# Optimization experiments

Measured on AMD Instinct MI355X. Metric: run time of the kernel, lower is better.

## Reference

```python
import jax, jax.numpy as jnp
import numpy as np

N, INC, INN, OUTC, OUTN, MAXD = 16, 32, 65536, 32, 8192, 16

def setup_inputs() -> dict:
    key = jax.random.key(0)
    ks = jax.random.split(key, 7)
    x = jax.random.normal(ks[0], (N, INC, INN), jnp.float32)
    A = jax.random.randint(ks[1], (OUTN, MAXD), 0, INN, dtype=jnp.int64)
    weight = 0.2 * jax.random.normal(ks[2], (INC, INN), jnp.float32)
    # normalize=True with fixed degree MAXD -> mask = 1/maxD everywhere
    mask = jnp.ones((OUTN, MAXD, 1), jnp.float32) / MAXD
    mask_weight = 0.2 * jax.random.normal(ks[3], (OUTN, MAXD, 1), jnp.float32)
    ct_weight = jax.random.normal(ks[4], (OUTC, INC), jnp.float32) / np.sqrt(INC)
    ct_bias = 0.02 * jax.random.normal(ks[5], (OUTC,), jnp.float32)
    bias = 0.2 * jax.random.normal(ks[6], (OUTC, OUTN), jnp.float32)
    return {"x": x, "A": A, "weight": weight, "mask": mask,
            "mask_weight": mask_weight, "ct_weight": ct_weight,
            "ct_bias": ct_bias, "bias": bias}

def reference(x, A, weight, mask, mask_weight, ct_weight, ct_bias, bias):
    n, inc, inn = x.shape
    outn, maxD = A.shape
    # per-input-node channel scaling, then lay out as (inn, N*inc) feature table
    feat = (x * weight).reshape(n * inc, inn).T            # (inn, N*inc)
    emb = feat[A]                                          # (outn, maxD, N*inc) gather
    w = mask_weight * mask                                 # (outn, maxD, 1)
    pooled = (w * emb).reshape(outn, maxD, n, inc).sum(axis=1)  # (outn, N, inc)
    almost_y = jnp.einsum('onc,dc->ond', pooled, ct_weight) + ct_bias  # (outn, N, outc)
    return almost_y.transpose(1, 2, 0) + bias              # (N, outc, outn)
```

## Files before the change

### kernel.cpp

```cpp
#include <hip/hip_runtime.h>
#include <hip/hip_bf16.h>

#define NN    16
#define INC   32
#define INN   65536
#define OUTC  32
#define OUTN  8192
#define MAXD  16
#define NC    512

typedef __attribute__((ext_vector_type(8))) unsigned short ushort8;
typedef __attribute__((ext_vector_type(4))) float f32x4;

__global__ __launch_bounds__(256) void transpose_scale_kernel(
    const float* __restrict__ x,
    const float* __restrict__ weight,
    unsigned short* __restrict__ feat)
{
    __shared__ float tile[64][65];
    const int l  = threadIdx.x;
    const int j0 = blockIdx.x * 64;
    const int r0 = blockIdx.y * 64;

    #pragma unroll
    for (int it = 0; it < 4; ++it) {
        int idx = it * 256 + l;
        int rl  = idx >> 4;
        int jj  = idx & 15;
        int r   = r0 + rl;
        int c   = r & 31;
        int j   = j0 + jj * 4;
        f32x4 xv = __builtin_nontemporal_load(
            reinterpret_cast<const f32x4*>(x + (size_t)r * INN + j));
        f32x4 wv = *reinterpret_cast<const f32x4*>(weight + (size_t)c * INN + j);
        tile[jj * 4 + 0][rl] = xv[0] * wv[0];
        tile[jj * 4 + 1][rl] = xv[1] * wv[1];
        tile[jj * 4 + 2][rl] = xv[2] * wv[2];
        tile[jj * 4 + 3][rl] = xv[3] * wv[3];
    }
    __syncthreads();

    #pragma unroll
    for (int p = 0; p < 2; ++p) {
        int jl = p * 32 + (l >> 3);
        int rs = (l & 7) * 8;
        ushort8 pk;
        #pragma unroll
        for (int k = 0; k < 8; ++k) {
            float v = tile[jl][rs + k];
            pk[k] = __bfloat16_as_ushort(__float2bfloat16(v));
        }
        *reinterpret_cast<ushort8*>(
            feat + (size_t)(j0 + jl) * NC + r0 + rs) = pk;
    }
}

#define OTILE 16

__global__ __launch_bounds__(512, 4) void gather_gemm_kernel(
    const unsigned short* __restrict__ feat,
    const int*   __restrict__ A,
    const float* __restrict__ mask,
    const float* __restrict__ mw,
    const float* __restrict__ ctw,
    const float* __restrict__ ctb,
    const float* __restrict__ bias,
    float*       __restrict__ out)
{
    __shared__ float pooled[OTILE][NC];
    __shared__ int   A_l[OTILE * MAXD];
    __shared__ float w_l[OTILE * MAXD];
    __shared__ float bias_l[32 * OTILE];

    const int l    = threadIdx.x;
    const int wave = l >> 6;
    const int lane = l & 63;
    const int o0   = blockIdx.x * OTILE;

    if (l < OTILE * MAXD) {
        A_l[l] = A[o0 * MAXD + l] & (INN - 1);
        w_l[l] = mw[o0 * MAXD + l] * mask[o0 * MAXD + l];
    }
    {
        int dout = l >> 4, o = l & 15;
        bias_l[l] = bias[(size_t)dout * OUTN + o0 + o];
    }
    __syncthreads();

    #pragma unroll
    for (int i = 0; i < 2; ++i) {
        const int o = wave + 8 * i;
        float acc[8] = {0.f, 0.f, 0.f, 0.f, 0.f, 0.f, 0.f, 0.f};
        #pragma unroll
        for (int d = 0; d < MAXD; ++d) {
            int   j  = A_l[o * MAXD + d];
            float wv = w_l[o * MAXD + d];
            ushort8 p = *reinterpret_cast<const ushort8*>(
                feat + (size_t)j * NC + lane * 8);
            #pragma unroll
            for (int k = 0; k < 8; ++k)
                acc[k] += wv * __uint_as_float((unsigned)p[k] << 16);
        }
        *reinterpret_cast<f32x4*>(&pooled[o][lane * 4]) =
            f32x4{acc[0], acc[1], acc[2], acc[3]};
        *reinterpret_cast<f32x4*>(&pooled[o][256 + lane * 4]) =
            f32x4{acc[4], acc[5], acc[6], acc[7]};
    }
    __syncthreads();

    const int dout = l & 31;
    const int n    = l >> 5;
    const float cb = ctb[dout];
    float vals[OTILE];
    #pragma unroll
    for (int o = 0; o < OTILE; ++o) vals[o] = cb + bias_l[dout * OTILE + o];

    #pragma unroll
    for (int q = 0; q < 8; ++q) {
        f32x4 cw = *reinterpret_cast<const f32x4*>(ctw + dout * 32 + 4 * q);
        const int sbase = (q & 1) * 256 + n * 16 + 4 * (q >> 1);
        #pragma unroll
        for (int o = 0; o < OTILE; ++o) {
            f32x4 pv = *reinterpret_cast<const f32x4*>(&pooled[o][sbase]);
            vals[o] += pv[0] * cw[0] + pv[1] * cw[1] + pv[2] * cw[2] + pv[3] * cw[3];
        }
    }

    float* orow = out + ((size_t)(n * 32 + dout)) * OUTN + o0;
    #pragma unroll
    for (int qq = 0; qq < 4; ++qq) {
        __builtin_nontemporal_store(
            f32x4{vals[4*qq], vals[4*qq+1], vals[4*qq+2], vals[4*qq+3]},
            reinterpret_cast<f32x4*>(orow + 4 * qq));
    }
}

extern "C" void kernel_launch(void* const* d_in, const int* in_sizes, int n_in,
                              void* d_out, int out_size, void* d_ws, size_t ws_size,
                              hipStream_t stream)
{
    const float* x      = (const float*)d_in[0];
    const int*   A      = (const int*)  d_in[1];
    const float* weight = (const float*)d_in[2];
    const float* mask   = (const float*)d_in[3];
    const float* mw     = (const float*)d_in[4];
    const float* ctw    = (const float*)d_in[5];
    const float* ctb    = (const float*)d_in[6];
    const float* bias   = (const float*)d_in[7];
    float* out = (float*)d_out;

    unsigned short* feat = (unsigned short*)d_ws;

    dim3 gA(INN / 64, NC / 64);
    transpose_scale_kernel<<<gA, 256, 0, stream>>>(x, weight, feat);

    gather_gemm_kernel<<<OUTN / OTILE, 512, 0, stream>>>(
        feat, A, mask, mw, ctw, ctb, bias, out);
}
```

Before: 258.8 us.

## Fuse transpose and gather-GEMM into one cooperative kernel with grid sync

Merges the transpose/scale pass and the gather-pool-GEMM pass into a single persistent cooperative kernel of 256 blocks. A grid-wide sync separates the two phases, and the two phases share one LDS union. The aim is to remove the second kernel launch and the gap between launches. In exchange the grid is much smaller, with one block per CU and 512 threads, so there is less latency hiding than the original 8192-block grid had. The two-kernel path is kept as a fallback if the cooperative launch fails.

```diff
diff --git a/kernel.cpp b/kernel.cpp
--- a/kernel.cpp
+++ b/kernel.cpp
@@ -1,5 +1,8 @@
 #include <hip/hip_runtime.h>
 #include <hip/hip_bf16.h>
+#include <hip/hip_cooperative_groups.h>
+
+namespace cg = cooperative_groups;
 
 #define NN    16
 #define INC   32
@@ -8,9 +11,145 @@
 #define OUTN  8192
 #define MAXD  16
 #define NC    512
+#define OTILE 16
+#define NBLK  256
 
 typedef __attribute__((ext_vector_type(8))) unsigned short ushort8;
 typedef __attribute__((ext_vector_type(4))) float f32x4;
+
+struct SMem {
+    union {
+        float tile[64][65];
+        float pooled[OTILE][NC];
+    } u;
+    int   A_l[OTILE * MAXD];
+    float w_l[OTILE * MAXD];
+    float bias_l[32 * OTILE];
+};
+
+__global__ __launch_bounds__(512, 2) void fused_kernel(
+    const float* __restrict__ x,
+    const float* __restrict__ weight,
+    const int*   __restrict__ A,
+    const float* __restrict__ mask,
+    const float* __restrict__ mw,
+    const float* __restrict__ ctw,
+    const float* __restrict__ ctb,
+    const float* __restrict__ bias,
+    unsigned short* __restrict__ feat,
+    float*       __restrict__ out)
+{
+    __shared__ SMem s;
+    const int l    = threadIdx.x;
+    const int bid  = blockIdx.x;
+    const int wave = l >> 6;
+    const int lane = l & 63;
+
+    #pragma unroll
+    for (int jt = 0; jt < 4; ++jt) {
+        const int j0 = bid * 256 + jt * 64;
+        for (int rc = 0; rc < 8; ++rc) {
+            const int r0 = rc * 64;
+            #pragma unroll
+            for (int it = 0; it < 2; ++it) {
+                int idx = it * 512 + l;
+                int rl  = idx >> 4;
+                int jj  = idx & 15;
+                int r   = r0 + rl;
+                int c   = r & 31;
+                int j   = j0 + jj * 4;
+                f32x4 xv = __builtin_nontemporal_load(
+                    reinterpret_cast<const f32x4*>(x + (size_t)r * INN + j));
+                f32x4 wv = *reinterpret_cast<const f32x4*>(
+                    weight + (size_t)c * INN + j);
+                s.u.tile[jj * 4 + 0][rl] = xv[0] * wv[0];
+                s.u.tile[jj * 4 + 1][rl] = xv[1] * wv[1];
+                s.u.tile[jj * 4 + 2][rl] = xv[2] * wv[2];
+                s.u.tile[jj * 4 + 3][rl] = xv[3] * wv[3];
+            }
+            __syncthreads();
+            {
+                int jl = l >> 3;
+                int rs = (l & 7) * 8;
+                ushort8 pk;
+                #pragma unroll
+                for (int k = 0; k < 8; ++k) {
+                    float v = s.u.tile[jl][rs + k];
+                    pk[k] = __bfloat16_as_ushort(__float2bfloat16(v));
+                }
+                *reinterpret_cast<ushort8*>(
+                    feat + (size_t)(j0 + jl) * NC + r0 + rs) = pk;
+            }
+            __syncthreads();
+        }
+    }
+
+    __threadfence();
+    cg::this_grid().sync();
+
+    for (int g = 0; g < 2; ++g) {
+        const int o0 = bid * 32 + g * OTILE;
+
+        if (l < OTILE * MAXD) {
+            s.A_l[l] = A[o0 * MAXD + l] & (INN - 1);
+            s.w_l[l] = mw[o0 * MAXD + l] * mask[o0 * MAXD + l];
+        }
+        {
+            int dout = l >> 4, o = l & 15;
+            s.bias_l[l] = bias[(size_t)dout * OUTN + o0 + o];
+        }
+        __syncthreads();
+
+        #pragma unroll
+        for (int i = 0; i < 2; ++i) {
+            const int o = wave + 8 * i;
+            float acc[8] = {0.f, 0.f, 0.f, 0.f, 0.f, 0.f, 0.f, 0.f};
+            #pragma unroll
+            for (int d = 0; d < MAXD; ++d) {
+                int   j  = s.A_l[o * MAXD + d];
+                float wv = s.w_l[o * MAXD + d];
+                ushort8 p = *reinterpret_cast<const ushort8*>(
+                    feat + (size_t)j * NC + lane * 8);
+                #pragma unroll
+                for (int k = 0; k < 8; ++k)
+                    acc[k] += wv * __uint_as_float((unsigned)p[k] << 16);
+            }
+            *reinterpret_cast<f32x4*>(&s.u.pooled[o][lane * 4]) =
+                f32x4{acc[0], acc[1], acc[2], acc[3]};
+            *reinterpret_cast<f32x4*>(&s.u.pooled[o][256 + lane * 4]) =
+                f32x4{acc[4], acc[5], acc[6], acc[7]};
+        }
+        __syncthreads();
+
+        const int dout = l & 31;
+        const int n    = l >> 5;
+        const float cb = ctb[dout];
+        float vals[OTILE];
+        #pragma unroll
+        for (int o = 0; o < OTILE; ++o)
+            vals[o] = cb + s.bias_l[dout * OTILE + o];
+
+        #pragma unroll
+        for (int q = 0; q < 8; ++q) {
+            f32x4 cw = *reinterpret_cast<const f32x4*>(ctw + dout * 32 + 4 * q);
+            const int sbase = (q & 1) * 256 + n * 16 + 4 * (q >> 1);
+            #pragma unroll
+            for (int o = 0; o < OTILE; ++o) {
+                f32x4 pv = *reinterpret_cast<const f32x4*>(&s.u.pooled[o][sbase]);
+                vals[o] += pv[0]*cw[0] + pv[1]*cw[1] + pv[2]*cw[2] + pv[3]*cw[3];
+            }
+        }
+
+        float* orow = out + ((size_t)(n * 32 + dout)) * OUTN + o0;
+        #pragma unroll
+        for (int qq = 0; qq < 4; ++qq) {
+            __builtin_nontemporal_store(
+                f32x4{vals[4*qq], vals[4*qq+1], vals[4*qq+2], vals[4*qq+3]},
+                reinterpret_cast<f32x4*>(orow + 4 * qq));
+        }
+        __syncthreads();
+    }
+}
 
 __global__ __launch_bounds__(256) void transpose_scale_kernel(
     const float* __restrict__ x,
@@ -55,8 +194,6 @@
     }
 }
 
-#define OTILE 16
-
 __global__ __launch_bounds__(512, 4) void gather_gemm_kernel(
     const unsigned short* __restrict__ feat,
     const int*   __restrict__ A,
@@ -122,7 +259,7 @@
         #pragma unroll
         for (int o = 0; o < OTILE; ++o) {
             f32x4 pv = *reinterpret_cast<const f32x4*>(&pooled[o][sbase]);
-            vals[o] += pv[0] * cw[0] + pv[1] * cw[1] + pv[2] * cw[2] + pv[3] * cw[3];
+            vals[o] += pv[0]*cw[0] + pv[1]*cw[1] + pv[2]*cw[2] + pv[3]*cw[3];
         }
     }
 
@@ -151,9 +288,17 @@
 
     unsigned short* feat = (unsigned short*)d_ws;
 
-    dim3 gA(INN / 64, NC / 64);
-    transpose_scale_kernel<<<gA, 256, 0, stream>>>(x, weight, feat);
-
-    gather_gemm_kernel<<<OUTN / OTILE, 512, 0, stream>>>(
-        feat, A, mask, mw, ctw, ctb, bias, out);
+    void* args[] = {
+        (void*)&x, (void*)&weight, (void*)&A, (void*)&mask, (void*)&mw,
+        (void*)&ctw, (void*)&ctb, (void*)&bias, (void*)&feat, (void*)&out
+    };
+    hipError_t err = hipLaunchCooperativeKernel(
+        (const void*)fused_kernel, dim3(NBLK), dim3(512), args, 0, stream);
+
+    if (err != hipSuccess) {
+        dim3 gA(INN / 64, NC / 64);
+        transpose_scale_kernel<<<gA, 256, 0, stream>>>(x, weight, feat);
+        gather_gemm_kernel<<<OUTN / OTILE, 512, 0, stream>>>(
+            feat, A, mask, mw, ctw, ctb, bias, out);
+    }
 }
```

Result: slower. 360.8 us (+39.4%).
